# Optimization experiments

Hardware: AMD Instinct MI355X
Metric: run time of the kernel (lower is better)

Reference implementation:

```python
import jax, jax.numpy as jnp
import numpy as np


def setup_inputs() -> dict:
    key = jax.random.key(0)
    k1, k2 = jax.random.split(key)
    n_task, shot, feat, n_class = 32, 2048, 1024, 512
    inputs = jax.random.normal(k1, (n_task, shot, feat), dtype=jnp.float32)
    weights = jax.random.normal(k2, (n_task, n_class, feat), dtype=jnp.float32)
    return {"inputs": inputs, "weights": weights, "temp": 15}


def reference(inputs, weights, temp):
    # logits[t,s,c] = temp * (x.w - 0.5*||w||^2 - 0.5*||x||^2)
    dots = jnp.einsum('tsf,tcf->tsc', inputs, weights)        # [T,S,C]
    w_sq = 0.5 * jnp.sum(weights * weights, axis=2)           # [T,C]
    x_sq = 0.5 * jnp.sum(inputs * inputs, axis=2)             # [T,S]
    logits = temp * (dots - w_sq[:, None, :] - x_sq[:, :, None])
    return jnp.argmax(logits, axis=2)                         # [T,S] int
```

## Files before the change

### kernel.cpp

```cpp
#include <hip/hip_runtime.h>
#include <cstdint>
#include <cstddef>

#define T_TASKS 32
#define S_SHOT  2048
#define F_FEAT  1024
#define C_CLS   512
#define MARGIN  0.1f
#define NBLK    (T_TASKS * (S_SHOT / 64))

typedef _Float16 f16;
typedef _Float16 f16x4 __attribute__((ext_vector_type(4)));
typedef _Float16 f16x8 __attribute__((ext_vector_type(8)));
typedef float    f32x4 __attribute__((ext_vector_type(4)));

__device__ __forceinline__ void gl_lds16(const void* g, void* l) {
  auto gp = (const __attribute__((address_space(1))) uint32_t*)(g);
  auto lp = (__attribute__((address_space(3))) uint32_t*)(l);
  __builtin_amdgcn_global_load_lds(gp, lp, 16, 0, 0);
}

__device__ __forceinline__ void upd3(float v, int i,
                                     float& v1, int& i1,
                                     float& v2, int& i2,
                                     float& v3, int& i3) {
  if (v > v1 || (v == v1 && i < i1)) { v3=v2; i3=i2; v2=v1; i2=i1; v1=v; i1=i; }
  else if (v > v2 || (v == v2 && i < i2)) { v3=v2; i3=i2; v2=v; i2=i; }
  else if (v > v3 || (v == v3 && i < i3)) { v3=v; i3=i; }
}

__global__ __launch_bounds__(256) void prep_w(const float* __restrict__ W,
                                              f16* __restrict__ Wh,
                                              float* __restrict__ wsq) {
  int rid = blockIdx.x * 4 + (threadIdx.x >> 6);
  int ln  = threadIdx.x & 63;
  int c   = rid & (C_CLS - 1);
  int t   = rid >> 9;
  const float* wr = W + (size_t)rid * F_FEAT;
  double s = 0.0;
#pragma unroll
  for (int j = 0; j < 4; ++j) {
    int f = (j * 64 + ln) * 4;
    float4 v = *(const float4*)(wr + f);
    s += (double)v.x * v.x + (double)v.y * v.y +
         (double)v.z * v.z + (double)v.w * v.w;
    f16x4 h;
    h.x = (f16)v.x; h.y = (f16)v.y; h.z = (f16)v.z; h.w = (f16)v.w;
    int kt = f >> 5;
    int q  = (f >> 3) & 3;
    int jj = f & 7;
    int u  = c * 4 + ((q + (c >> 1)) & 3);
    size_t off = ((size_t)(t * 32 + kt) << 14) + (size_t)u * 8 + jj;
    *(f16x4*)(Wh + off) = h;
  }
#pragma unroll
  for (int off = 32; off > 0; off >>= 1) s += __shfl_xor(s, off);
  if (ln == 0) wsq[rid] = (float)(0.5 * s);
}

struct MainSh {
  f16 W0[16384];
  f16 W1[16384];
};
struct EpiSh {
  float  swsq[C_CLS];
  float  cv[64][2][3];
  int    ci[64][2][3];
  double rs[48];
  int    amb_cnt;
  int    amb_list[64];
};
union ShU { MainSh m; EpiSh e; };

__device__ __forceinline__ void issue_w8(const f16* Wht, f16* dst, int ktn,
                                         int wv, int ln) {
  const f16* g = Wht + ((size_t)ktn << 14) + wv * 4096 + ln * 8;
  f16* l = dst + wv * 4096;
#pragma unroll
  for (int i = 0; i < 8; ++i) gl_lds16(g + i * 512, l + i * 512);
}

__device__ __forceinline__ void cvt8(float4 u, float4 v, f16x8& h, f16x8& l) {
  h[0] = (f16)u.x; l[0] = (f16)(u.x - (float)h[0]);
  h[1] = (f16)u.y; l[1] = (f16)(u.y - (float)h[1]);
  h[2] = (f16)u.z; l[2] = (f16)(u.z - (float)h[2]);
  h[3] = (f16)u.w; l[3] = (f16)(u.w - (float)h[3]);
  h[4] = (f16)v.x; l[4] = (f16)(v.x - (float)h[4]);
  h[5] = (f16)v.y; l[5] = (f16)(v.y - (float)h[5]);
  h[6] = (f16)v.z; l[6] = (f16)(v.z - (float)h[6]);
  h[7] = (f16)v.w; l[7] = (f16)(v.w - (float)h[7]);
}

__global__ __launch_bounds__(256, 2) void gemm_argmax(
    const float* __restrict__ X, const float* __restrict__ W,
    const f16* __restrict__ Wh, const float* __restrict__ wsq,
    int* __restrict__ out) {
  __shared__ __align__(16) ShU sh;

  const int tid = threadIdx.x;
  const int wv  = tid >> 6, ln = tid & 63;
  const int rg  = wv >> 1, cg = wv & 1;
  const int m   = ln & 15, q = ln >> 4;

  int bx = blockIdx.x;
  bx = (bx & 7) * (NBLK / 8) + (bx >> 3);
  const int t    = bx >> 5, rb = bx & 31;
  const int row0 = rb * 64;

  const f16* Wht = Wh + ((size_t)(t * 32) << 14);

  const float* xgA = X + ((size_t)(t * S_SHOT) + row0 + rg * 32 + m) * F_FEAT + q * 8;
  const float* xgB = xgA + (size_t)16 * F_FEAT;

  const int c0 = cg * 256 + m;
  const int u0 = c0 * 4 + ((q + (c0 >> 1)) & 3);

  const f32x4 zero4 = {0.f, 0.f, 0.f, 0.f};
  f32x4 acc[2][16];
#pragma unroll
  for (int a = 0; a < 2; ++a)
#pragma unroll
    for (int b = 0; b < 16; ++b) acc[a][b] = zero4;

  issue_w8(Wht, sh.m.W0, 0, wv, ln);
  float4 xa0 = *(const float4*)(xgA);
  float4 xa1 = *(const float4*)(xgA + 4);
  float4 xb0 = *(const float4*)(xgB);
  float4 xb1 = *(const float4*)(xgB + 4);

#define KSTEP(KT, WRD, WST, PRED)                                            \
  {                                                                          \
    __syncthreads();                                                         \
    const bool pr_ = (PRED);                                                 \
    if (pr_) issue_w8(Wht, (WST), (KT) + 1, wv, ln);                         \
    float4 na0, na1, nb0, nb1;                                               \
    if (pr_) {                                                               \
      const float* pA_ = xgA + ((KT) + 1) * 32;                              \
      const float* pB_ = xgB + ((KT) + 1) * 32;                              \
      na0 = *(const float4*)(pA_); na1 = *(const float4*)(pA_ + 4);          \
      nb0 = *(const float4*)(pB_); nb1 = *(const float4*)(pB_ + 4);          \
    }                                                                        \
    f16x8 ah0, al0, ah1, al1;                                                \
    cvt8(xa0, xa1, ah0, al0);                                                \
    cvt8(xb0, xb1, ah1, al1);                                                \
    __builtin_amdgcn_s_setprio(1);                                           \
    const f16* bp_ = (WRD) + u0 * 8;                                         \
    _Pragma("unroll")                                                        \
    for (int ct = 0; ct < 16; ++ct) {                                        \
      f16x8 bh = *(const f16x8*)(bp_ + ct * 512);                            \
      acc[0][ct] = __builtin_amdgcn_mfma_f32_16x16x32_f16(ah0, bh, acc[0][ct], 0, 0, 0); \
      acc[0][ct] = __builtin_amdgcn_mfma_f32_16x16x32_f16(al0, bh, acc[0][ct], 0, 0, 0); \
      acc[1][ct] = __builtin_amdgcn_mfma_f32_16x16x32_f16(ah1, bh, acc[1][ct], 0, 0, 0); \
      acc[1][ct] = __builtin_amdgcn_mfma_f32_16x16x32_f16(al1, bh, acc[1][ct], 0, 0, 0); \
    }                                                                        \
    __builtin_amdgcn_s_setprio(0);                                           \
    if (pr_) { xa0 = na0; xa1 = na1; xb0 = nb0; xb1 = nb1; }                 \
  }

#pragma unroll 1
  for (int kp = 0; kp < 16; ++kp) {
    KSTEP(2 * kp,     sh.m.W0, sh.m.W1, true);
    KSTEP(2 * kp + 1, sh.m.W1, sh.m.W0, kp < 15);
  }
#undef KSTEP

  __syncthreads();

  sh.e.swsq[tid]       = wsq[t * C_CLS + tid];
  sh.e.swsq[tid + 256] = wsq[t * C_CLS + tid + 256];
  if (tid == 0) sh.e.amb_cnt = 0;
  __syncthreads();

#pragma unroll
  for (int rt = 0; rt < 2; ++rt) {
#pragma unroll
    for (int rr = 0; rr < 4; ++rr) {
      float v1 = -3.4e38f, v2 = -3.4e38f, v3 = -3.4e38f;
      int   i1 = 0x7fffffff, i2 = 0x7fffffff, i3 = 0x7fffffff;
#pragma unroll
      for (int ct = 0; ct < 16; ++ct) {
        int cidx = c0 + ct * 16;
        float sc = acc[rt][ct][rr] - sh.e.swsq[cidx];
        upd3(sc, cidx, v1, i1, v2, i2, v3, i3);
      }
      for (int off = 1; off < 16; off <<= 1) {
        float w1 = __shfl_xor(v1, off); int j1 = __shfl_xor(i1, off);
        float w2 = __shfl_xor(v2, off); int j2 = __shfl_xor(i2, off);
        float w3 = __shfl_xor(v3, off); int j3 = __shfl_xor(i3, off);
        upd3(w1, j1, v1, i1, v2, i2, v3, i3);
        upd3(w2, j2, v1, i1, v2, i2, v3, i3);
        upd3(w3, j3, v1, i1, v2, i2, v3, i3);
      }
      if (m == 0) {
        int row = rg * 32 + rt * 16 + q * 4 + rr;
        sh.e.cv[row][cg][0] = v1; sh.e.ci[row][cg][0] = i1;
        sh.e.cv[row][cg][1] = v2; sh.e.ci[row][cg][1] = i2;
        sh.e.cv[row][cg][2] = v3; sh.e.ci[row][cg][2] = i3;
      }
    }
  }
  __syncthreads();

  if (tid < 64) {
    float a1 = sh.e.cv[tid][0][0]; int aj = sh.e.ci[tid][0][0];
    float b1 = sh.e.cv[tid][1][0]; int bj = sh.e.ci[tid][1][0];
    float win, runner; int widx;
    if (a1 > b1 || (a1 == b1 && aj < bj)) {
      win = a1; widx = aj; runner = fmaxf(b1, sh.e.cv[tid][0][1]);
    } else {
      win = b1; widx = bj; runner = fmaxf(a1, sh.e.cv[tid][1][1]);
    }
    if (win - runner >= MARGIN) {
      out[t * S_SHOT + row0 + tid] = widx;
    } else {
      int p = atomicAdd(&sh.e.amb_cnt, 1);
      sh.e.amb_list[p] = tid;
    }
  }
  __syncthreads();

  int nA = sh.e.amb_cnt;
  for (int base = 0; base < nA; base += 8) {
    int nr = nA - base; if (nr > 8) nr = 8;
    int np = nr * 6;
    for (int p = wv; p < np; p += 4) {
      int rrow = p / 6;
      int cand = p - rrow * 6;
      int rl   = sh.e.amb_list[base + rrow];
      int g    = (cand >= 3) ? 1 : 0;
      int k    = cand - g * 3;
      int cidx = sh.e.ci[rl][g][k];
      const float* xr = X + ((size_t)t * S_SHOT + row0 + rl) * F_FEAT;
      const float* wr = W + ((size_t)t * C_CLS + cidx) * F_FEAT;
      double sd = 0.0, sw = 0.0;
#pragma unroll
      for (int j = 0; j < 16; ++j) {
        float xv  = xr[ln + 64 * j];
        float wv2 = wr[ln + 64 * j];
        sd += (double)xv * (double)wv2;
        sw += (double)wv2 * (double)wv2;
      }
#pragma unroll
      for (int off = 32; off > 0; off >>= 1) {
        sd += __shfl_xor(sd, off);
        sw += __shfl_xor(sw, off);
      }
      if (ln == 0) sh.e.rs[p] = sd - 0.5 * sw;
    }
    __syncthreads();
    if (tid < nr) {
      int rl = sh.e.amb_list[base + tid];
      double best = -1.0e300; int bidx = 0x7fffffff;
#pragma unroll
      for (int cand = 0; cand < 6; ++cand) {
        int g = cand / 3, k = cand % 3;
        int cidx = sh.e.ci[rl][g][k];
        double sc = sh.e.rs[tid * 6 + cand];
        if (sc > best || (sc == best && cidx < bidx)) { best = sc; bidx = cidx; }
      }
      out[t * S_SHOT + row0 + rl] = bidx;
    }
    __syncthreads();
  }
}

extern "C" void kernel_launch(void* const* d_in, const int* in_sizes, int n_in,
                              void* d_out, int out_size, void* d_ws, size_t ws_size,
                              hipStream_t stream) {
  (void)in_sizes; (void)n_in; (void)out_size;
  const float* X = (const float*)d_in[0];
  const float* W = (const float*)d_in[1];
  const size_t wh_bytes = (size_t)T_TASKS * C_CLS * F_FEAT * sizeof(f16);
  const size_t need = wh_bytes + (size_t)T_TASKS * C_CLS * sizeof(float);
  if (ws_size < need) return;
  f16*   Wh  = (f16*)d_ws;
  float* wsq = (float*)((char*)d_ws + wh_bytes);
  int*   out = (int*)d_out;
  prep_w<<<T_TASKS * C_CLS / 4, 256, 0, stream>>>(W, Wh, wsq);
  gemm_argmax<<<NBLK, 256, 0, stream>>>(X, W, Wh, wsq, out);
}
```

Measured before the change: 824.3 us.

## Grow row tile to 256 with 1024-thread blocks and coalesce the fp16 weight prep

Each block now covers 256 input rows with 16 waves sharing one double-buffered fp16 weight tile. That cuts repeated weight loads from L2/HBM by a factor of four, and each wave issues only two async LDS loads per k-step. The per-k-step __syncthreads is replaced by an explicit vmcnt wait on the weight loads plus s_barrier, so the prefetched X loads stay in flight. Weight prep is split into a norm kernel and an LDS-staged, coalesced fp16 transpose kernel. The trade-offs are fewer, larger blocks, a launch bound of one block per CU with tighter register limits, and an extra kernel launch.

```diff
diff --git a/kernel.cpp b/kernel.cpp
--- a/kernel.cpp
+++ b/kernel.cpp
@@ -7,7 +7,8 @@
 #define F_FEAT  1024
 #define C_CLS   512
 #define MARGIN  0.1f
-#define NBLK    (T_TASKS * (S_SHOT / 64))
+#define BM      256
+#define NBLK    (T_TASKS * (S_SHOT / BM))
 
 typedef _Float16 f16;
 typedef _Float16 f16x4 __attribute__((ext_vector_type(4)));
@@ -29,13 +30,10 @@
   else if (v > v3 || (v == v3 && i < i3)) { v3=v; i3=i; }
 }
 
-__global__ __launch_bounds__(256) void prep_w(const float* __restrict__ W,
-                                              f16* __restrict__ Wh,
-                                              float* __restrict__ wsq) {
+__global__ __launch_bounds__(256) void prep_wsq(const float* __restrict__ W,
+                                                float* __restrict__ wsq) {
   int rid = blockIdx.x * 4 + (threadIdx.x >> 6);
   int ln  = threadIdx.x & 63;
-  int c   = rid & (C_CLS - 1);
-  int t   = rid >> 9;
   const float* wr = W + (size_t)rid * F_FEAT;
   double s = 0.0;
 #pragma unroll
@@ -44,18 +42,38 @@
     float4 v = *(const float4*)(wr + f);
     s += (double)v.x * v.x + (double)v.y * v.y +
          (double)v.z * v.z + (double)v.w * v.w;
+  }
+#pragma unroll
+  for (int off = 32; off > 0; off >>= 1) s += __shfl_xor(s, off);
+  if (ln == 0) wsq[rid] = (float)(0.5 * s);
+}
+
+__global__ __launch_bounds__(256) void prep_wh(const float* __restrict__ W,
+                                               f16* __restrict__ Wh) {
+  __shared__ __align__(16) f16 tile[16384];
+  const int bid = blockIdx.x;
+  const int t   = bid >> 5, kt = bid & 31;
+  const int tid = threadIdx.x;
+  const int cr  = tid >> 3;
+  const int q4  = tid & 7;
+  const float* base = W + (size_t)t * C_CLS * F_FEAT + kt * 32 + q4 * 4;
+#pragma unroll
+  for (int rr = 0; rr < 16; ++rr) {
+    int c = rr * 32 + cr;
+    float4 v = *(const float4*)(base + (size_t)c * F_FEAT);
     f16x4 h;
     h.x = (f16)v.x; h.y = (f16)v.y; h.z = (f16)v.z; h.w = (f16)v.w;
-    int kt = f >> 5;
-    int q  = (f >> 3) & 3;
-    int jj = f & 7;
-    int u  = c * 4 + ((q + (c >> 1)) & 3);
-    size_t off = ((size_t)(t * 32 + kt) << 14) + (size_t)u * 8 + jj;
-    *(f16x4*)(Wh + off) = h;
-  }
-#pragma unroll
-  for (int off = 32; off > 0; off >>= 1) s += __shfl_xor(s, off);
-  if (ln == 0) wsq[rid] = (float)(0.5 * s);
+    int u  = c * 4 + (((q4 >> 1) + (c >> 1)) & 3);
+    int jj = (q4 & 1) * 4;
+    *(f16x4*)(tile + u * 8 + jj) = h;
+  }
+  __syncthreads();
+  f16* dst = Wh + ((size_t)bid << 14);
+#pragma unroll
+  for (int i = 0; i < 8; ++i) {
+    *(f16x8*)(dst + i * 2048 + tid * 8) =
+        *(const f16x8*)(tile + i * 2048 + tid * 8);
+  }
 }
 
 struct MainSh {
@@ -64,20 +82,20 @@
 };
 struct EpiSh {
   float  swsq[C_CLS];
-  float  cv[64][2][3];
-  int    ci[64][2][3];
-  double rs[48];
+  float  cv[BM][2][3];
+  int    ci[BM][2][3];
+  double rs[96];
   int    amb_cnt;
-  int    amb_list[64];
+  int    amb_list[BM];
 };
 union ShU { MainSh m; EpiSh e; };
 
-__device__ __forceinline__ void issue_w8(const f16* Wht, f16* dst, int ktn,
+__device__ __forceinline__ void issue_w2(const f16* Wht, f16* dst, int ktn,
                                          int wv, int ln) {
-  const f16* g = Wht + ((size_t)ktn << 14) + wv * 4096 + ln * 8;
-  f16* l = dst + wv * 4096;
-#pragma unroll
-  for (int i = 0; i < 8; ++i) gl_lds16(g + i * 512, l + i * 512);
+  const f16* g = Wht + ((size_t)ktn << 14) + wv * 1024 + ln * 8;
+  f16* l = dst + wv * 1024;
+  gl_lds16(g, l);
+  gl_lds16(g + 512, l + 512);
 }
 
 __device__ __forceinline__ void cvt8(float4 u, float4 v, f16x8& h, f16x8& l) {
@@ -91,7 +109,7 @@
   h[7] = (f16)v.w; l[7] = (f16)(v.w - (float)h[7]);
 }
 
-__global__ __launch_bounds__(256, 2) void gemm_argmax(
+__global__ __launch_bounds__(1024, 1) void gemm_argmax(
     const float* __restrict__ X, const float* __restrict__ W,
     const f16* __restrict__ Wh, const float* __restrict__ wsq,
     int* __restrict__ out) {
@@ -104,8 +122,8 @@
 
   int bx = blockIdx.x;
   bx = (bx & 7) * (NBLK / 8) + (bx >> 3);
-  const int t    = bx >> 5, rb = bx & 31;
-  const int row0 = rb * 64;
+  const int t    = bx >> 3, rb = bx & 7;
+  const int row0 = rb * BM;
 
   const f16* Wht = Wh + ((size_t)(t * 32) << 14);
 
@@ -122,17 +140,24 @@
 #pragma unroll
     for (int b = 0; b < 16; ++b) acc[a][b] = zero4;
 
-  issue_w8(Wht, sh.m.W0, 0, wv, ln);
+  issue_w2(Wht, sh.m.W0, 0, wv, ln);
+  __builtin_amdgcn_sched_barrier(0);
   float4 xa0 = *(const float4*)(xgA);
   float4 xa1 = *(const float4*)(xgA + 4);
   float4 xb0 = *(const float4*)(xgB);
   float4 xb1 = *(const float4*)(xgB + 4);
+  __builtin_amdgcn_sched_barrier(0);
+  asm volatile("s_waitcnt vmcnt(4)" ::: "memory");
+  __builtin_amdgcn_sched_barrier(0);
+  __builtin_amdgcn_s_barrier();
 
 #define KSTEP(KT, WRD, WST, PRED)                                            \
   {                                                                          \
-    __syncthreads();                                                         \
     const bool pr_ = (PRED);                                                 \
-    if (pr_) issue_w8(Wht, (WST), (KT) + 1, wv, ln);                         \
+    if (pr_) {                                                               \
+      issue_w2(Wht, (WST), (KT) + 1, wv, ln);                                \
+      __builtin_amdgcn_sched_barrier(0);                                     \
+    }                                                                        \
     float4 na0, na1, nb0, nb1;                                               \
     if (pr_) {                                                               \
       const float* pA_ = xgA + ((KT) + 1) * 32;                              \
@@ -155,6 +180,12 @@
     }                                                                        \
     __builtin_amdgcn_s_setprio(0);                                           \
     if (pr_) { xa0 = na0; xa1 = na1; xb0 = nb0; xb1 = nb1; }                 \
+    if (pr_) {                                                               \
+      __builtin_amdgcn_sched_barrier(0);                                     \
+      asm volatile("s_waitcnt vmcnt(4)" ::: "memory");  \
+      __builtin_amdgcn_sched_barrier(0);                                     \
+    }                                                                        \
+    __builtin_amdgcn_s_barrier();                                            \
   }
 
 #pragma unroll 1
@@ -166,8 +197,7 @@
 
   __syncthreads();
 
-  sh.e.swsq[tid]       = wsq[t * C_CLS + tid];
-  sh.e.swsq[tid + 256] = wsq[t * C_CLS + tid + 256];
+  if (tid < C_CLS) sh.e.swsq[tid] = wsq[t * C_CLS + tid];
   if (tid == 0) sh.e.amb_cnt = 0;
   __syncthreads();
 
@@ -201,7 +231,7 @@
   }
   __syncthreads();
 
-  if (tid < 64) {
+  if (tid < BM) {
     float a1 = sh.e.cv[tid][0][0]; int aj = sh.e.ci[tid][0][0];
     float b1 = sh.e.cv[tid][1][0]; int bj = sh.e.ci[tid][1][0];
     float win, runner; int widx;
@@ -220,10 +250,10 @@
   __syncthreads();
 
   int nA = sh.e.amb_cnt;
-  for (int base = 0; base < nA; base += 8) {
-    int nr = nA - base; if (nr > 8) nr = 8;
+  for (int base = 0; base < nA; base += 16) {
+    int nr = nA - base; if (nr > 16) nr = 16;
     int np = nr * 6;
-    for (int p = wv; p < np; p += 4) {
+    for (int p = wv; p < np; p += 16) {
       int rrow = p / 6;
       int cand = p - rrow * 6;
       int rl   = sh.e.amb_list[base + rrow];
@@ -276,6 +306,7 @@
   f16*   Wh  = (f16*)d_ws;
   float* wsq = (float*)((char*)d_ws + wh_bytes);
   int*   out = (int*)d_out;
-  prep_w<<<T_TASKS * C_CLS / 4, 256, 0, stream>>>(W, Wh, wsq);
-  gemm_argmax<<<NBLK, 256, 0, stream>>>(X, W, Wh, wsq, out);
-}
+  prep_wsq<<<T_TASKS * C_CLS / 4, 256, 0, stream>>>(W, wsq);
+  prep_wh<<<T_TASKS * 32, 256, 0, stream>>>(W, Wh);
+  gemm_argmax<<<NBLK, 1024, 0, stream>>>(X, W, Wh, wsq, out);
+}
```

After: 1.511 ms. 83.3% more time.

## Read fp16 weights directly from global memory and transpose via LDS tile

Applied to the files above, without the earlier changes.

The GEMM kernel stops staging weight tiles through double-buffered LDS with global_load_lds and block barriers. Each wave now loads its B fragments straight from the pre-swizzled fp16 weight buffer in global memory and relies on cache for reuse across waves. The weight prep is split into a norm kernel and a layout kernel that builds each swizzled 32-column tile in LDS, so its global writes become coalesced. The GEMM drops its per-step barriers and LDS pressure, but every wave now issues global loads with their latency exposed, and there is one extra kernel launch.

```diff
diff --git a/kernel.cpp b/kernel.cpp
--- a/kernel.cpp
+++ b/kernel.cpp
@@ -13,12 +13,6 @@
 typedef _Float16 f16x4 __attribute__((ext_vector_type(4)));
 typedef _Float16 f16x8 __attribute__((ext_vector_type(8)));
 typedef float    f32x4 __attribute__((ext_vector_type(4)));
-
-__device__ __forceinline__ void gl_lds16(const void* g, void* l) {
-  auto gp = (const __attribute__((address_space(1))) uint32_t*)(g);
-  auto lp = (__attribute__((address_space(3))) uint32_t*)(l);
-  __builtin_amdgcn_global_load_lds(gp, lp, 16, 0, 0);
-}
 
 __device__ __forceinline__ void upd3(float v, int i,
                                      float& v1, int& i1,
@@ -29,13 +23,10 @@
   else if (v > v3 || (v == v3 && i < i3)) { v3=v; i3=i; }
 }
 
-__global__ __launch_bounds__(256) void prep_w(const float* __restrict__ W,
-                                              f16* __restrict__ Wh,
-                                              float* __restrict__ wsq) {
+__global__ __launch_bounds__(256) void prep_wsq(const float* __restrict__ W,
+                                                float* __restrict__ wsq) {
   int rid = blockIdx.x * 4 + (threadIdx.x >> 6);
   int ln  = threadIdx.x & 63;
-  int c   = rid & (C_CLS - 1);
-  int t   = rid >> 9;
   const float* wr = W + (size_t)rid * F_FEAT;
   double s = 0.0;
 #pragma unroll
@@ -44,24 +35,40 @@
     float4 v = *(const float4*)(wr + f);
     s += (double)v.x * v.x + (double)v.y * v.y +
          (double)v.z * v.z + (double)v.w * v.w;
+  }
+#pragma unroll
+  for (int off = 32; off > 0; off >>= 1) s += __shfl_xor(s, off);
+  if (ln == 0) wsq[rid] = (float)(0.5 * s);
+}
+
+__global__ __launch_bounds__(256) void prep_wh(const float* __restrict__ W,
+                                               f16* __restrict__ Wh) {
+  __shared__ __align__(16) f16 tile[16384];
+  const int bid = blockIdx.x;
+  const int t   = bid >> 5, kt = bid & 31;
+  const int tid = threadIdx.x;
+  const int cr  = tid >> 3;
+  const int q4  = tid & 7;
+  const float* base = W + (size_t)t * C_CLS * F_FEAT + kt * 32 + q4 * 4;
+#pragma unroll
+  for (int rr = 0; rr < 16; ++rr) {
+    int c = rr * 32 + cr;
+    float4 v = *(const float4*)(base + (size_t)c * F_FEAT);
     f16x4 h;
     h.x = (f16)v.x; h.y = (f16)v.y; h.z = (f16)v.z; h.w = (f16)v.w;
-    int kt = f >> 5;
-    int q  = (f >> 3) & 3;
-    int jj = f & 7;
-    int u  = c * 4 + ((q + (c >> 1)) & 3);
-    size_t off = ((size_t)(t * 32 + kt) << 14) + (size_t)u * 8 + jj;
-    *(f16x4*)(Wh + off) = h;
-  }
-#pragma unroll
-  for (int off = 32; off > 0; off >>= 1) s += __shfl_xor(s, off);
-  if (ln == 0) wsq[rid] = (float)(0.5 * s);
-}
-
-struct MainSh {
-  f16 W0[16384];
-  f16 W1[16384];
-};
+    int u  = c * 4 + (((q4 >> 1) + (c >> 1)) & 3);
+    int jj = (q4 & 1) * 4;
+    *(f16x4*)(tile + u * 8 + jj) = h;
+  }
+  __syncthreads();
+  f16* dst = Wh + ((size_t)bid << 14);
+#pragma unroll
+  for (int i = 0; i < 8; ++i) {
+    *(f16x8*)(dst + i * 2048 + tid * 8) =
+        *(const f16x8*)(tile + i * 2048 + tid * 8);
+  }
+}
+
 struct EpiSh {
   float  swsq[C_CLS];
   float  cv[64][2][3];
@@ -70,15 +77,6 @@
   int    amb_cnt;
   int    amb_list[64];
 };
-union ShU { MainSh m; EpiSh e; };
-
-__device__ __forceinline__ void issue_w8(const f16* Wht, f16* dst, int ktn,
-                                         int wv, int ln) {
-  const f16* g = Wht + ((size_t)ktn << 14) + wv * 4096 + ln * 8;
-  f16* l = dst + wv * 4096;
-#pragma unroll
-  for (int i = 0; i < 8; ++i) gl_lds16(g + i * 512, l + i * 512);
-}
 
 __device__ __forceinline__ void cvt8(float4 u, float4 v, f16x8& h, f16x8& l) {
   h[0] = (f16)u.x; l[0] = (f16)(u.x - (float)h[0]);
@@ -95,7 +93,7 @@
     const float* __restrict__ X, const float* __restrict__ W,
     const f16* __restrict__ Wh, const float* __restrict__ wsq,
     int* __restrict__ out) {
-  __shared__ __align__(16) ShU sh;
+  __shared__ __align__(16) EpiSh sh;
 
   const int tid = threadIdx.x;
   const int wv  = tid >> 6, ln = tid & 63;
@@ -107,14 +105,13 @@
   const int t    = bx >> 5, rb = bx & 31;
   const int row0 = rb * 64;
 
-  const f16* Wht = Wh + ((size_t)(t * 32) << 14);
+  const int c0 = cg * 256 + m;
+  const int u0 = c0 * 4 + ((q + (c0 >> 1)) & 3);
+  const f16* Wb = Wh + ((size_t)(t * 32) << 14) + (size_t)u0 * 8;
 
   const float* xgA = X + ((size_t)(t * S_SHOT) + row0 + rg * 32 + m) * F_FEAT + q * 8;
   const float* xgB = xgA + (size_t)16 * F_FEAT;
 
-  const int c0 = cg * 256 + m;
-  const int u0 = c0 * 4 + ((q + (c0 >> 1)) & 3);
-
   const f32x4 zero4 = {0.f, 0.f, 0.f, 0.f};
   f32x4 acc[2][16];
 #pragma unroll
@@ -122,53 +119,47 @@
 #pragma unroll
     for (int b = 0; b < 16; ++b) acc[a][b] = zero4;
 
-  issue_w8(Wht, sh.m.W0, 0, wv, ln);
   float4 xa0 = *(const float4*)(xgA);
   float4 xa1 = *(const float4*)(xgA + 4);
   float4 xb0 = *(const float4*)(xgB);
   float4 xb1 = *(const float4*)(xgB + 4);
 
-#define KSTEP(KT, WRD, WST, PRED)                                            \
-  {                                                                          \
-    __syncthreads();                                                         \
-    const bool pr_ = (PRED);                                                 \
-    if (pr_) issue_w8(Wht, (WST), (KT) + 1, wv, ln);                         \
-    float4 na0, na1, nb0, nb1;                                               \
-    if (pr_) {                                                               \
-      const float* pA_ = xgA + ((KT) + 1) * 32;                              \
-      const float* pB_ = xgB + ((KT) + 1) * 32;                              \
-      na0 = *(const float4*)(pA_); na1 = *(const float4*)(pA_ + 4);          \
-      nb0 = *(const float4*)(pB_); nb1 = *(const float4*)(pB_ + 4);          \
-    }                                                                        \
-    f16x8 ah0, al0, ah1, al1;                                                \
-    cvt8(xa0, xa1, ah0, al0);                                                \
-    cvt8(xb0, xb1, ah1, al1);                                                \
-    __builtin_amdgcn_s_setprio(1);                                           \
-    const f16* bp_ = (WRD) + u0 * 8;                                         \
-    _Pragma("unroll")                                                        \
-    for (int ct = 0; ct < 16; ++ct) {                                        \
-      f16x8 bh = *(const f16x8*)(bp_ + ct * 512);                            \
-      acc[0][ct] = __builtin_amdgcn_mfma_f32_16x16x32_f16(ah0, bh, acc[0][ct], 0, 0, 0); \
-      acc[0][ct] = __builtin_amdgcn_mfma_f32_16x16x32_f16(al0, bh, acc[0][ct], 0, 0, 0); \
-      acc[1][ct] = __builtin_amdgcn_mfma_f32_16x16x32_f16(ah1, bh, acc[1][ct], 0, 0, 0); \
-      acc[1][ct] = __builtin_amdgcn_mfma_f32_16x16x32_f16(al1, bh, acc[1][ct], 0, 0, 0); \
-    }                                                                        \
-    __builtin_amdgcn_s_setprio(0);                                           \
-    if (pr_) { xa0 = na0; xa1 = na1; xb0 = nb0; xb1 = nb1; }                 \
-  }
-
 #pragma unroll 1
-  for (int kp = 0; kp < 16; ++kp) {
-    KSTEP(2 * kp,     sh.m.W0, sh.m.W1, true);
-    KSTEP(2 * kp + 1, sh.m.W1, sh.m.W0, kp < 15);
-  }
-#undef KSTEP
-
-  __syncthreads();
-
-  sh.e.swsq[tid]       = wsq[t * C_CLS + tid];
-  sh.e.swsq[tid + 256] = wsq[t * C_CLS + tid + 256];
-  if (tid == 0) sh.e.amb_cnt = 0;
+  for (int kt = 0; kt < 32; ++kt) {
+    float4 na0, na1, nb0, nb1;
+    if (kt < 31) {
+      const float* pA_ = xgA + (kt + 1) * 32;
+      const float* pB_ = xgB + (kt + 1) * 32;
+      na0 = *(const float4*)(pA_); na1 = *(const float4*)(pA_ + 4);
+      nb0 = *(const float4*)(pB_); nb1 = *(const float4*)(pB_ + 4);
+    }
+    f16x8 ah0, al0, ah1, al1;
+    cvt8(xa0, xa1, ah0, al0);
+    cvt8(xb0, xb1, ah1, al1);
+
+    const f16* bp = Wb + ((size_t)kt << 14);
+#pragma unroll
+    for (int ct = 0; ct < 8; ++ct) {
+      f16x8 bh = *(const f16x8*)(bp + ct * 512);
+      acc[0][ct] = __builtin_amdgcn_mfma_f32_16x16x32_f16(ah0, bh, acc[0][ct], 0, 0, 0);
+      acc[0][ct] = __builtin_amdgcn_mfma_f32_16x16x32_f16(al0, bh, acc[0][ct], 0, 0, 0);
+      acc[1][ct] = __builtin_amdgcn_mfma_f32_16x16x32_f16(ah1, bh, acc[1][ct], 0, 0, 0);
+      acc[1][ct] = __builtin_amdgcn_mfma_f32_16x16x32_f16(al1, bh, acc[1][ct], 0, 0, 0);
+    }
+#pragma unroll
+    for (int ct = 8; ct < 16; ++ct) {
+      f16x8 bh = *(const f16x8*)(bp + ct * 512);
+      acc[0][ct] = __builtin_amdgcn_mfma_f32_16x16x32_f16(ah0, bh, acc[0][ct], 0, 0, 0);
+      acc[0][ct] = __builtin_amdgcn_mfma_f32_16x16x32_f16(al0, bh, acc[0][ct], 0, 0, 0);
+      acc[1][ct] = __builtin_amdgcn_mfma_f32_16x16x32_f16(ah1, bh, acc[1][ct], 0, 0, 0);
+      acc[1][ct] = __builtin_amdgcn_mfma_f32_16x16x32_f16(al1, bh, acc[1][ct], 0, 0, 0);
+    }
+    xa0 = na0; xa1 = na1; xb0 = nb0; xb1 = nb1;
+  }
+
+  sh.swsq[tid]       = wsq[t * C_CLS + tid];
+  sh.swsq[tid + 256] = wsq[t * C_CLS + tid + 256];
+  if (tid == 0) sh.amb_cnt = 0;
   __syncthreads();
 
 #pragma unroll
@@ -180,7 +171,7 @@
 #pragma unroll
       for (int ct = 0; ct < 16; ++ct) {
         int cidx = c0 + ct * 16;
-        float sc = acc[rt][ct][rr] - sh.e.swsq[cidx];
+        float sc = acc[rt][ct][rr] - sh.swsq[cidx];
         upd3(sc, cidx, v1, i1, v2, i2, v3, i3);
       }
       for (int off = 1; off < 16; off <<= 1) {
@@ -193,43 +184,43 @@
       }
       if (m == 0) {
         int row = rg * 32 + rt * 16 + q * 4 + rr;
-        sh.e.cv[row][cg][0] = v1; sh.e.ci[row][cg][0] = i1;
-        sh.e.cv[row][cg][1] = v2; sh.e.ci[row][cg][1] = i2;
-        sh.e.cv[row][cg][2] = v3; sh.e.ci[row][cg][2] = i3;
+        sh.cv[row][cg][0] = v1; sh.ci[row][cg][0] = i1;
+        sh.cv[row][cg][1] = v2; sh.ci[row][cg][1] = i2;
+        sh.cv[row][cg][2] = v3; sh.ci[row][cg][2] = i3;
       }
     }
   }
   __syncthreads();
 
   if (tid < 64) {
-    float a1 = sh.e.cv[tid][0][0]; int aj = sh.e.ci[tid][0][0];
-    float b1 = sh.e.cv[tid][1][0]; int bj = sh.e.ci[tid][1][0];
+    float a1 = sh.cv[tid][0][0]; int aj = sh.ci[tid][0][0];
+    float b1 = sh.cv[tid][1][0]; int bj = sh.ci[tid][1][0];
     float win, runner; int widx;
     if (a1 > b1 || (a1 == b1 && aj < bj)) {
-      win = a1; widx = aj; runner = fmaxf(b1, sh.e.cv[tid][0][1]);
+      win = a1; widx = aj; runner = fmaxf(b1, sh.cv[tid][0][1]);
     } else {
-      win = b1; widx = bj; runner = fmaxf(a1, sh.e.cv[tid][1][1]);
+      win = b1; widx = bj; runner = fmaxf(a1, sh.cv[tid][1][1]);
     }
     if (win - runner >= MARGIN) {
       out[t * S_SHOT + row0 + tid] = widx;
     } else {
-      int p = atomicAdd(&sh.e.amb_cnt, 1);
-      sh.e.amb_list[p] = tid;
-    }
-  }
-  __syncthreads();
-
-  int nA = sh.e.amb_cnt;
+      int p = atomicAdd(&sh.amb_cnt, 1);
+      sh.amb_list[p] = tid;
+    }
+  }
+  __syncthreads();
+
+  int nA = sh.amb_cnt;
   for (int base = 0; base < nA; base += 8) {
     int nr = nA - base; if (nr > 8) nr = 8;
     int np = nr * 6;
     for (int p = wv; p < np; p += 4) {
       int rrow = p / 6;
       int cand = p - rrow * 6;
-      int rl   = sh.e.amb_list[base + rrow];
+      int rl   = sh.amb_list[base + rrow];
       int g    = (cand >= 3) ? 1 : 0;
       int k    = cand - g * 3;
-      int cidx = sh.e.ci[rl][g][k];
+      int cidx = sh.ci[rl][g][k];
       const float* xr = X + ((size_t)t * S_SHOT + row0 + rl) * F_FEAT;
       const float* wr = W + ((size_t)t * C_CLS + cidx) * F_FEAT;
       double sd = 0.0, sw = 0.0;
@@ -245,17 +236,17 @@
         sd += __shfl_xor(sd, off);
         sw += __shfl_xor(sw, off);
       }
-      if (ln == 0) sh.e.rs[p] = sd - 0.5 * sw;
+      if (ln == 0) sh.rs[p] = sd - 0.5 * sw;
     }
     __syncthreads();
     if (tid < nr) {
-      int rl = sh.e.amb_list[base + tid];
+      int rl = sh.amb_list[base + tid];
       double best = -1.0e300; int bidx = 0x7fffffff;
 #pragma unroll
       for (int cand = 0; cand < 6; ++cand) {
         int g = cand / 3, k = cand % 3;
-        int cidx = sh.e.ci[rl][g][k];
-        double sc = sh.e.rs[tid * 6 + cand];
+        int cidx = sh.ci[rl][g][k];
+        double sc = sh.rs[tid * 6 + cand];
         if (sc > best || (sc == best && cidx < bidx)) { best = sc; bidx = cidx; }
       }
       out[t * S_SHOT + row0 + rl] = bidx;
@@ -276,6 +267,7 @@
   f16*   Wh  = (f16*)d_ws;
   float* wsq = (float*)((char*)d_ws + wh_bytes);
   int*   out = (int*)d_out;
-  prep_w<<<T_TASKS * C_CLS / 4, 256, 0, stream>>>(W, Wh, wsq);
+  prep_wsq<<<T_TASKS * C_CLS / 4, 256, 0, stream>>>(W, wsq);
+  prep_wh<<<T_TASKS * 32, 256, 0, stream>>>(W, Wh);
   gemm_argmax<<<NBLK, 256, 0, stream>>>(X, W, Wh, wsq, out);
 }
```

After: 892.3 us. 8.2% more time.
